# Optimization experiments

Hardware: AMD Instinct MI355X
Metric: run time of the kernel (lower is better)

## Reference

```python
import math
import jax, jax.numpy as jnp
import numpy as np

NUM_HEADS = 32
NUM_KV_HEADS = 8
HEAD_DIM = 128
HIDDEN = 4096
ROPE_THETA = 500000.0
ROPE_FACTOR = 8.0
HIGH_FF = 4.0
LOW_FF = 1.0
ORIG_MAX_POS = 8192


def _llama3_inv_freq():
    # Llama-3 rope frequency scaling
    inv = 1.0 / (ROPE_THETA ** (np.arange(0, HEAD_DIM, 2, dtype=np.float32) / HEAD_DIM))
    wavelen = 2.0 * np.pi / inv
    low_wl = ORIG_MAX_POS / LOW_FF
    high_wl = ORIG_MAX_POS / HIGH_FF
    inv_scaled = np.where(wavelen > low_wl, inv / ROPE_FACTOR, inv)
    smooth = (ORIG_MAX_POS / wavelen - LOW_FF) / (HIGH_FF - LOW_FF)
    smoothed = (1.0 - smooth) / ROPE_FACTOR * inv + smooth * inv
    is_medium = (wavelen <= low_wl) & (wavelen >= high_wl)
    return jnp.asarray(np.where(is_medium, smoothed, inv_scaled), dtype=jnp.float32)


def _rotate_half(x):
    h = x.shape[-1] // 2
    return jnp.concatenate([-x[..., h:], x[..., :h]], axis=-1)


def setup_inputs() -> dict:
    key = jax.random.key(0)
    ks = jax.random.split(key, 5)
    s = 0.02
    return {
        "x": jax.random.normal(ks[0], (1, 2048, HIDDEN), dtype=jnp.float32),
        "Wq": jax.random.normal(ks[1], (NUM_HEADS * HEAD_DIM, HIDDEN), dtype=jnp.float32) * s,
        "Wk": jax.random.normal(ks[2], (NUM_KV_HEADS * HEAD_DIM, HIDDEN), dtype=jnp.float32) * s,
        "Wv": jax.random.normal(ks[3], (NUM_KV_HEADS * HEAD_DIM, HIDDEN), dtype=jnp.float32) * s,
        "Wo": jax.random.normal(ks[4], (HIDDEN, NUM_HEADS * HEAD_DIM), dtype=jnp.float32) * s,
    }


def reference(x, Wq, Wk, Wv, Wo):
    B, T, _ = x.shape
    G = NUM_HEADS // NUM_KV_HEADS  # query heads per kv head

    q = jnp.einsum("bth,oh->bto", x, Wq).reshape(B, T, NUM_HEADS, HEAD_DIM).transpose(0, 2, 1, 3)
    k = jnp.einsum("bth,oh->bto", x, Wk).reshape(B, T, NUM_KV_HEADS, HEAD_DIM).transpose(0, 2, 1, 3)
    v = jnp.einsum("bth,oh->bto", x, Wv).reshape(B, T, NUM_KV_HEADS, HEAD_DIM).transpose(0, 2, 1, 3)

    # RoPE (past_len = 0, prefill)
    inv_freq = _llama3_inv_freq()
    pos = jnp.arange(T, dtype=jnp.float32)
    freqs = pos[:, None] * inv_freq[None, :]             # [T, D/2]
    emb = jnp.concatenate([freqs, freqs], axis=-1)       # [T, D]
    cos, sin = jnp.cos(emb), jnp.sin(emb)
    q = q * cos + _rotate_half(q) * sin
    k = k * cos + _rotate_half(k) * sin

    # GQA attention: group query heads over kv heads instead of repeat_interleave
    qg = q.reshape(B, NUM_KV_HEADS, G, T, HEAD_DIM)
    scale = 1.0 / math.sqrt(HEAD_DIM)
    scores = jnp.einsum("bkgtd,bksd->bkgts", qg, k) * scale  # [B,Hkv,G,T,T]
    causal = jnp.tril(jnp.ones((T, T), dtype=bool))
    scores = jnp.where(causal, scores, -jnp.inf)
    attn = jax.nn.softmax(scores, axis=-1)
    out = jnp.einsum("bkgts,bksd->bkgtd", attn, v)           # [B,Hkv,G,T,D]
    out = out.reshape(B, NUM_HEADS, T, HEAD_DIM).transpose(0, 2, 1, 3).reshape(B, T, NUM_HEADS * HEAD_DIM)
    return jnp.einsum("bto,ho->bth", out, Wo)
```

## Files before the change

### kernel.cpp

```cpp
#include <hip/hip_runtime.h>
#include <math.h>

#define T 2048
#define HID 4096
#define NH 32
#define NKV 8
#define HD 128
#define QSCALE 0.08838834764831845f

typedef __attribute__((ext_vector_type(8))) short short8;
typedef __attribute__((ext_vector_type(4))) float f32x4;
typedef __attribute__((ext_vector_type(16))) float f32x16;

static __device__ __forceinline__ unsigned short f2bf(float f) {
  union { float f; unsigned u; } v; v.f = f;
  unsigned r = v.u;
  r += 0x7fffu + ((r >> 16) & 1u);
  return (unsigned short)(r >> 16);
}

static __device__ __forceinline__ void async_cp16(const unsigned short* g, unsigned short* l) {
  __builtin_amdgcn_global_load_lds(
      (const __attribute__((address_space(1))) void*)g,
      (__attribute__((address_space(3))) void*)l,
      16, 0, 0);
}

__global__ __launch_bounds__(256) void cast4_kernel(const float* __restrict__ s0, const float* __restrict__ s1,
                                                    const float* __restrict__ s2, const float* __restrict__ s3,
                                                    unsigned short* __restrict__ d0, unsigned short* __restrict__ d1,
                                                    unsigned short* __restrict__ d2, unsigned short* __restrict__ d3,
                                                    int n0, int n1, int n2, int n3) {
  int i = blockIdx.x * 256 + threadIdx.x;
  const float* s; unsigned short* d; int j = i;
  if (j < n0) { s = s0; d = d0; }
  else { j -= n0;
    if (j < n1) { s = s1; d = d1; }
    else { j -= n1;
      if (j < n2) { s = s2; d = d2; }
      else { j -= n2;
        if (j >= n3) return;
        s = s3; d = d3; } } }
  float4 f = ((const float4*)s)[j];
  ushort4 o;
  o.x = f2bf(f.x); o.y = f2bf(f.y); o.z = f2bf(f.z); o.w = f2bf(f.w);
  ((ushort4*)d)[j] = o;
}

__global__ __launch_bounds__(256) void cast_bf16_kernel(const float* __restrict__ src,
                                                        unsigned short* __restrict__ dst,
                                                        int n4) {
  int i = blockIdx.x * 256 + threadIdx.x;
  if (i >= n4) return;
  float4 f = ((const float4*)src)[i];
  ushort4 o;
  o.x = f2bf(f.x); o.y = f2bf(f.y); o.z = f2bf(f.z); o.w = f2bf(f.w);
  ((ushort4*)dst)[i] = o;
}


static __device__ __forceinline__ short8 ldfrag(const unsigned short* tile, int row0, int ks, int lane) {
  int row = row0 + (lane & 15);
  int slot = (ks * 4 + (lane >> 4)) ^ (lane & 7);
  return *(const short8*)&tile[row * 64 + slot * 8];
}

static __device__ __forceinline__ void stage_half(const unsigned short* __restrict__ G, long grow0, int K, int k0,
                                                  unsigned short* lds, int h, int wave, int lane) {
#pragma unroll
  for (int i = 0; i < 2; i++) {
    long row = grow0 + h * 128 + i * 64 + wave * 8 + (lane >> 3);
    int slot = (lane & 7) ^ (lane >> 3);
    async_cp16(&G[row * (long)K + k0 + slot * 8], &lds[h * 8192 + i * 4096 + wave * 512]);
  }
}

template <int MQ, int NQ>
static __device__ __forceinline__ void mfma_quad(const short8 (&af)[4][2], const short8 (&bf)[2][2],
                                                 f32x4 (&acc)[8][4]) {
  __builtin_amdgcn_s_setprio(1);
#pragma unroll
  for (int m = 0; m < 4; m++)
#pragma unroll
    for (int n = 0; n < 2; n++)
#pragma unroll
      for (int ks = 0; ks < 2; ks++)
        acc[MQ * 4 + m][NQ * 2 + n] = __builtin_amdgcn_mfma_f32_16x16x32_bf16(
            af[m][ks], bf[n][ks], acc[MQ * 4 + m][NQ * 2 + n], 0, 0, 0);
  __builtin_amdgcn_s_setprio(0);
}

#define SCHED0 __builtin_amdgcn_sched_barrier(0)
#define BAR_PRE  do { SCHED0; __builtin_amdgcn_s_barrier(); \
                      asm volatile("s_waitcnt lgkmcnt(0)" ::: "memory"); SCHED0; } while (0)
#define BAR_POST do { SCHED0; __builtin_amdgcn_s_barrier(); SCHED0; } while (0)

__global__ __launch_bounds__(512, 2) void gemm8(const unsigned short* __restrict__ A,
                                                const unsigned short* __restrict__ Bt,
                                                float* __restrict__ C,
                                                int M, int N, int K) {
  __shared__ __align__(16) unsigned short As[2][16384];
  __shared__ __align__(16) unsigned short Bs[2][16384];
  int tid = threadIdx.x, wave = tid >> 6, lane = tid & 63;
  int wm = wave >> 2, wn = wave & 3;
  long bm0 = (long)blockIdx.y * 256, bn0 = (long)blockIdx.x * 256;
  int ar = wm * 128, br = wn * 64;

  f32x4 acc[8][4] = {};
  short8 a0[4][2], a1[4][2], b0[2][2], b1[2][2];

  stage_half(Bt, bn0, K, 0, Bs[0], 0, wave, lane);
  stage_half(Bt, bn0, K, 0, Bs[0], 1, wave, lane);
  stage_half(A,  bm0, K, 0, As[0], 0, wave, lane);
  stage_half(A,  bm0, K, 0, As[0], 1, wave, lane);
  stage_half(Bt, bn0, K, 64, Bs[1], 0, wave, lane);
  stage_half(Bt, bn0, K, 64, Bs[1], 1, wave, lane);
  asm volatile("s_waitcnt vmcnt(4)" ::: "memory");
  SCHED0; __builtin_amdgcn_s_barrier(); SCHED0;

  int nkt = K >> 6;
#pragma unroll 1
  for (int it = 0; it < (nkt >> 1); ++it) {
    int k1 = (2 * it + 1) << 6;
    int t2 = 2 * it + 2; if (t2 > nkt - 1) t2 = nkt - 1;
    int t3 = 2 * it + 3; if (t3 > nkt - 1) t3 = nkt - 1;
    int k2 = t2 << 6, k3 = t3 << 6;

#pragma unroll
    for (int m = 0; m < 4; m++)
#pragma unroll
      for (int ks = 0; ks < 2; ks++) a0[m][ks] = ldfrag(As[0], ar + m * 16, ks, lane);
#pragma unroll
    for (int n = 0; n < 2; n++)
#pragma unroll
      for (int ks = 0; ks < 2; ks++) b0[n][ks] = ldfrag(Bs[0], br + n * 16, ks, lane);
    stage_half(A, bm0, K, k1, As[1], 0, wave, lane);
    BAR_PRE; mfma_quad<0, 0>(a0, b0, acc); BAR_POST;

#pragma unroll
    for (int n = 0; n < 2; n++)
#pragma unroll
      for (int ks = 0; ks < 2; ks++) b1[n][ks] = ldfrag(Bs[0], br + (2 + n) * 16, ks, lane);
    stage_half(A, bm0, K, k1, As[1], 1, wave, lane);
    BAR_PRE; mfma_quad<0, 1>(a0, b1, acc); BAR_POST;

#pragma unroll
    for (int m = 0; m < 4; m++)
#pragma unroll
      for (int ks = 0; ks < 2; ks++) a1[m][ks] = ldfrag(As[0], ar + (4 + m) * 16, ks, lane);
    stage_half(Bt, bn0, K, k2, Bs[0], 0, wave, lane);
    BAR_PRE; mfma_quad<1, 0>(a1, b0, acc); BAR_POST;

    stage_half(Bt, bn0, K, k2, Bs[0], 1, wave, lane);
    asm volatile("s_waitcnt vmcnt(4)" ::: "memory");
    BAR_PRE; mfma_quad<1, 1>(a1, b1, acc); BAR_POST;

#pragma unroll
    for (int m = 0; m < 4; m++)
#pragma unroll
      for (int ks = 0; ks < 2; ks++) a0[m][ks] = ldfrag(As[1], ar + m * 16, ks, lane);
#pragma unroll
    for (int n = 0; n < 2; n++)
#pragma unroll
      for (int ks = 0; ks < 2; ks++) b0[n][ks] = ldfrag(Bs[1], br + n * 16, ks, lane);
    stage_half(A, bm0, K, k2, As[0], 0, wave, lane);
    BAR_PRE; mfma_quad<0, 0>(a0, b0, acc); BAR_POST;

#pragma unroll
    for (int n = 0; n < 2; n++)
#pragma unroll
      for (int ks = 0; ks < 2; ks++) b1[n][ks] = ldfrag(Bs[1], br + (2 + n) * 16, ks, lane);
    stage_half(A, bm0, K, k2, As[0], 1, wave, lane);
    BAR_PRE; mfma_quad<0, 1>(a0, b1, acc); BAR_POST;

#pragma unroll
    for (int m = 0; m < 4; m++)
#pragma unroll
      for (int ks = 0; ks < 2; ks++) a1[m][ks] = ldfrag(As[1], ar + (4 + m) * 16, ks, lane);
    stage_half(Bt, bn0, K, k3, Bs[1], 0, wave, lane);
    BAR_PRE; mfma_quad<1, 0>(a1, b0, acc); BAR_POST;

    stage_half(Bt, bn0, K, k3, Bs[1], 1, wave, lane);
    asm volatile("s_waitcnt vmcnt(4)" ::: "memory");
    BAR_PRE; mfma_quad<1, 1>(a1, b1, acc); BAR_POST;
  }
  asm volatile("s_waitcnt vmcnt(0)" ::: "memory");

#pragma unroll
  for (int m = 0; m < 8; m++)
#pragma unroll
    for (int n = 0; n < 4; n++) {
      long row = bm0 + ar + m * 16 + ((lane >> 4) << 2);
      long col = bn0 + br + n * 16 + (lane & 15);
#pragma unroll
      for (int j = 0; j < 4; j++)
        C[(row + j) * (long)N + col] = acc[m][n][j];
    }
}

__global__ __launch_bounds__(64) void rope_qk(const float* __restrict__ qkvf,
                                              unsigned short* __restrict__ qb,
                                              unsigned short* __restrict__ kb) {
  int t = blockIdx.x, hh = blockIdx.y, d = threadIdx.x;
  float ex = (float)d * (1.0f / 64.0f);
  float inv = expf(-ex * 13.122363377404328f);
  float wl = 6.283185307179586f / inv;
  float inv_s;
  if (wl > 8192.0f)       inv_s = inv * 0.125f;
  else if (wl < 2048.0f)  inv_s = inv;
  else {
    float smooth = (8192.0f / wl - 1.0f) * (1.0f / 3.0f);
    inv_s = (1.0f - smooth) * 0.125f * inv + smooth * inv;
  }
  float ang = (float)t * inv_s;
  float s, c;
  sincosf(ang, &s, &c);
  if (hh < NH) {
    const float* base = qkvf + (long)t * 6144 + hh * HD;
    float lo = base[d], hi = base[d + 64];
    long o = ((long)hh * T + t) * HD;
    qb[o + d]      = f2bf((lo * c - hi * s) * QSCALE);
    qb[o + d + 64] = f2bf((hi * c + lo * s) * QSCALE);
  } else {
    int h = hh - NH;
    const float* base = qkvf + (long)t * 6144 + 4096 + h * HD;
    float lo = base[d], hi = base[d + 64];
    long o = ((long)h * T + t) * HD;
    kb[o + d]      = f2bf(lo * c - hi * s);
    kb[o + d + 64] = f2bf(hi * c + lo * s);
  }
}

__global__ __launch_bounds__(256) void transpose_v(const float* __restrict__ qkvf,
                                                   unsigned short* __restrict__ vtb) {
  __shared__ float tile[64][33];
  int t0 = blockIdx.x * 64, d0 = blockIdx.y * 32, h = blockIdx.z;
  int tid = threadIdx.x;
  int dd = tid & 31, tt = tid >> 5;
#pragma unroll
  for (int i = 0; i < 8; i++) {
    int t = tt + i * 8;
    tile[t][dd] = qkvf[(long)(t0 + t) * 6144 + 5120 + h * HD + d0 + dd];
  }
  __syncthreads();
  int t2 = tid & 63, d2 = tid >> 6;
#pragma unroll
  for (int i = 0; i < 8; i++) {
    int d = d2 + i * 4;
    vtb[((long)(h * HD + d0 + d)) * T + t0 + t2] = f2bf(tile[t2][d]);
  }
}

__global__ __launch_bounds__(256, 2) void attn_kernel(const unsigned short* __restrict__ qb,
                                                      const unsigned short* __restrict__ kbuf,
                                                      const unsigned short* __restrict__ vtb,
                                                      unsigned short* __restrict__ ob) {
  __shared__ __align__(16) unsigned short Ks[64 * 128];
  __shared__ __align__(16) unsigned short Vs[128 * 64];
  __shared__ __align__(16) unsigned short Ps[4][32 * 76];
  int h = blockIdx.y;
  int kvh = h >> 2;
  int qt = (blockIdx.y >= 16) ? (int)(gridDim.x - 1 - blockIdx.x) : (int)blockIdx.x;
  int q0 = qt * 128;
  int tid = threadIdx.x, wave = tid >> 6, lane = tid & 63;
  int l31 = lane & 31, half = lane >> 5;
  const unsigned short* Kb = kbuf + (long)kvh * T * HD;
  const unsigned short* Vb = vtb + (long)kvh * HD * T;

  int qrow = q0 + wave * 32 + l31;
  short8 aq[8];
#pragma unroll
  for (int ks = 0; ks < 8; ks++)
    aq[ks] = *(const short8*)&qb[((long)h * T + qrow) * HD + ks * 16 + half * 8];

  f32x16 oacc[4] = {};
  float psum[16];
#pragma unroll
  for (int r = 0; r < 16; r++) psum[r] = 0.0f;

  int ntiles = 2 * qt + 2;
  for (int tile = 0; tile < ntiles; tile++) {
    int kb0 = tile * 64;
#pragma unroll
    for (int i = 0; i < 4; i++) {
      int c = wave * 4 + i;
      { int row = c * 4 + (lane >> 4);
        int g = (lane & 15) ^ (row & 15);
        async_cp16(&Kb[(long)(kb0 + row) * HD + g * 8], &Ks[c * 512]); }
      { int row = c * 8 + (lane >> 3);
        int g = (lane & 7) ^ (row & 7);
        async_cp16(&Vb[(long)row * T + kb0 + g * 8], &Vs[c * 512]); }
    }
    __syncthreads();

    f32x16 sacc[2] = {};
#pragma unroll
    for (int ks = 0; ks < 8; ks++)
#pragma unroll
      for (int nt = 0; nt < 2; nt++) {
        int row = nt * 32 + l31;
        short8 bk = *(const short8*)&Ks[row * 128 + (((2 * ks + half) ^ (row & 15)) * 8)];
        sacc[nt] = __builtin_amdgcn_mfma_f32_32x32x16_bf16(aq[ks], bk, sacc[nt], 0, 0, 0);
      }

    if (kb0 + 63 > q0 + wave * 32) {
#pragma unroll
      for (int nt = 0; nt < 2; nt++) {
        int key = kb0 + nt * 32 + l31;
#pragma unroll
        for (int r = 0; r < 16; r++) {
          int qr = q0 + wave * 32 + (r & 3) + 8 * (r >> 2) + 4 * half;
          if (key > qr) sacc[nt][r] = -3.0e38f;
        }
      }
    }

#pragma unroll
    for (int nt = 0; nt < 2; nt++)
#pragma unroll
      for (int r = 0; r < 16; r++) {
        float p = __expf(sacc[nt][r]);
        psum[r] += p;
        int prow = (r & 3) + 8 * (r >> 2) + 4 * half;
        Ps[wave][prow * 76 + nt * 32 + l31] = f2bf(p);
      }

#pragma unroll
    for (int ks = 0; ks < 4; ks++) {
      short8 ap = *(const short8*)&Ps[wave][l31 * 76 + ks * 16 + half * 8];
#pragma unroll
      for (int nt = 0; nt < 4; nt++) {
        int row = nt * 32 + l31;
        short8 bv = *(const short8*)&Vs[row * 64 + (((2 * ks + half) ^ (row & 7)) * 8)];
        oacc[nt] = __builtin_amdgcn_mfma_f32_32x32x16_bf16(ap, bv, oacc[nt], 0, 0, 0);
      }
    }
    __syncthreads();
  }

#pragma unroll
  for (int off = 1; off <= 16; off <<= 1)
#pragma unroll
    for (int r = 0; r < 16; r++)
      psum[r] += __shfl_xor(psum[r], off, 64);

#pragma unroll
  for (int nt = 0; nt < 4; nt++)
#pragma unroll
    for (int r = 0; r < 16; r++) {
      int row = q0 + wave * 32 + (r & 3) + 8 * (r >> 2) + 4 * half;
      ob[(long)row * HID + h * HD + nt * 32 + l31] = f2bf(oacc[nt][r] / psum[r]);
    }
}

extern "C" void kernel_launch(void* const* d_in, const int* in_sizes, int n_in,
                              void* d_out, int out_size, void* d_ws, size_t ws_size,
                              hipStream_t stream) {
  const float* x  = (const float*)d_in[0];
  const float* Wq = (const float*)d_in[1];
  const float* Wk = (const float*)d_in[2];
  const float* Wv = (const float*)d_in[3];
  const float* Wo = (const float*)d_in[4];
  float* out = (float*)d_out;

  char* ws = (char*)d_ws;
  size_t off = 0;
  auto alloc = [&](size_t bytes) {
    char* p = ws + off;
    off += (bytes + 255) & ~(size_t)255;
    return p;
  };
  unsigned short* x_bf    = (unsigned short*)alloc((size_t)T * HID * 2);
  unsigned short* wqkv_bf = (unsigned short*)alloc((size_t)6144 * HID * 2);
  float* qkvf = (float*)alloc((size_t)T * 6144 * 4);
  unsigned short* qb  = (unsigned short*)alloc((size_t)NH * T * HD * 2);
  unsigned short* kbb = (unsigned short*)alloc((size_t)NKV * T * HD * 2);
  unsigned short* vtb = (unsigned short*)alloc((size_t)NKV * HD * T * 2);
  unsigned short* obb = (unsigned short*)alloc((size_t)T * HID * 2);

  int n0 = T * HID / 4, n1 = HID * HID / 4, n2 = 1024 * HID / 4, n3 = 1024 * HID / 4;
  int ntot = n0 + n1 + n2 + n3;
  cast4_kernel<<<dim3((ntot + 255) / 256), dim3(256), 0, stream>>>(
      x, Wq, Wk, Wv,
      x_bf, wqkv_bf, wqkv_bf + (size_t)HID * HID, wqkv_bf + (size_t)5120 * HID,
      n0, n1, n2, n3);

  gemm8<<<dim3(6144 / 256, T / 256), dim3(512), 0, stream>>>(x_bf, wqkv_bf, qkvf, T, 6144, HID);

  rope_qk<<<dim3(T, NH + NKV), dim3(64), 0, stream>>>(qkvf, qb, kbb);
  transpose_v<<<dim3(T / 64, HD / 32, NKV), dim3(256), 0, stream>>>(qkvf, vtb);

  cast_bf16_kernel<<<dim3((HID * HID / 4 + 255) / 256), dim3(256), 0, stream>>>(Wo, wqkv_bf, HID * HID / 4);
  attn_kernel<<<dim3(T / 128, NH), dim3(256), 0, stream>>>(qb, kbb, vtb, obb);
  gemm8<<<dim3(HID / 256, T / 256), dim3(512), 0, stream>>>(obb, wqkv_bf, out, T, HID, HID);
}
```

Measured before the change: 506.8 us.

## Narrow GEMM N-tiles to fill all CUs with templated pipeline

Templates the bf16 GEMM on the number of N fragments per wave, giving 192-wide tiles for the QKV projection and 128-wide tiles for the output projection. The grids become 256 workgroups, matching the CU count, where before the projections launched 192 and 128 workgroups and left CUs idle. The staging and MFMA phase schedule is rebuilt per tile width with new vmcnt waits. Smaller N tiles lower the reuse of each loaded A tile and increase total global/L2 traffic.

```diff
diff --git a/kernel.cpp b/kernel.cpp
--- a/kernel.cpp
+++ b/kernel.cpp
@@ -65,28 +65,43 @@
   return *(const short8*)&tile[row * 64 + slot * 8];
 }
 
-static __device__ __forceinline__ void stage_half(const unsigned short* __restrict__ G, long grow0, int K, int k0,
-                                                  unsigned short* lds, int h, int wave, int lane) {
-#pragma unroll
-  for (int i = 0; i < 2; i++) {
-    long row = grow0 + h * 128 + i * 64 + wave * 8 + (lane >> 3);
-    int slot = (lane & 7) ^ (lane >> 3);
-    async_cp16(&G[row * (long)K + k0 + slot * 8], &lds[h * 8192 + i * 4096 + wave * 512]);
-  }
-}
-
-template <int MQ, int NQ>
-static __device__ __forceinline__ void mfma_quad(const short8 (&af)[4][2], const short8 (&bf)[2][2],
-                                                 f32x4 (&acc)[8][4]) {
+static __device__ __forceinline__ void stage64(const unsigned short* __restrict__ G, long grow0, int K, int k0,
+                                               unsigned short* lds, int wave, int lane) {
+  long row = grow0 + wave * 8 + (lane >> 3);
+  int slot = (lane & 7) ^ (lane >> 3);
+  async_cp16(&G[row * (long)K + k0 + slot * 8], &lds[wave * 512]);
+}
+
+template <int MQ>
+static __device__ __forceinline__ void lda(short8 (&dst)[4][2], const unsigned short* tile, int ar, int lane) {
+#pragma unroll
+  for (int m = 0; m < 4; m++)
+#pragma unroll
+    for (int ks = 0; ks < 2; ks++)
+      dst[m][ks] = ldfrag(tile, ar + MQ * 64 + m * 16, ks, lane);
+}
+
+template <int N0, int NN, int NF>
+static __device__ __forceinline__ void ldb(short8 (&b)[NF][2], const unsigned short* tile, int br, int lane) {
+#pragma unroll
+  for (int n = 0; n < NN; n++)
+#pragma unroll
+    for (int ks = 0; ks < 2; ks++)
+      b[N0 + n][ks] = ldfrag(tile, br + (N0 + n) * 16, ks, lane);
+}
+
+template <int MQ, int N0, int NN, int NF>
+static __device__ __forceinline__ void mfma_ph(const short8 (&af)[4][2], const short8 (&b)[NF][2],
+                                               f32x4 (&acc)[8][NF]) {
   __builtin_amdgcn_s_setprio(1);
 #pragma unroll
-  for (int m = 0; m < 4; m++)
-#pragma unroll
-    for (int n = 0; n < 2; n++)
-#pragma unroll
-      for (int ks = 0; ks < 2; ks++)
-        acc[MQ * 4 + m][NQ * 2 + n] = __builtin_amdgcn_mfma_f32_16x16x32_bf16(
-            af[m][ks], bf[n][ks], acc[MQ * 4 + m][NQ * 2 + n], 0, 0, 0);
+  for (int ks = 0; ks < 2; ks++)
+#pragma unroll
+    for (int m = 0; m < 4; m++)
+#pragma unroll
+      for (int n = 0; n < NN; n++)
+        acc[MQ * 4 + m][N0 + n] = __builtin_amdgcn_mfma_f32_16x16x32_bf16(
+            af[m][ks], b[N0 + n][ks], acc[MQ * 4 + m][N0 + n], 0, 0, 0);
   __builtin_amdgcn_s_setprio(0);
 }
 
@@ -94,102 +109,116 @@
 #define BAR_PRE  do { SCHED0; __builtin_amdgcn_s_barrier(); \
                       asm volatile("s_waitcnt lgkmcnt(0)" ::: "memory"); SCHED0; } while (0)
 #define BAR_POST do { SCHED0; __builtin_amdgcn_s_barrier(); SCHED0; } while (0)
-
-__global__ __launch_bounds__(512, 2) void gemm8(const unsigned short* __restrict__ A,
-                                                const unsigned short* __restrict__ Bt,
-                                                float* __restrict__ C,
-                                                int M, int N, int K) {
+#define VMCNT(n) asm volatile("s_waitcnt vmcnt(" #n ")" ::: "memory")
+
+template <int NF>
+__global__ __launch_bounds__(512, 2) void gemm8t(const unsigned short* __restrict__ A,
+                                                 const unsigned short* __restrict__ Bt,
+                                                 float* __restrict__ C,
+                                                 int M, int N, int K) {
+  constexpr int BN = NF * 64;
   __shared__ __align__(16) unsigned short As[2][16384];
-  __shared__ __align__(16) unsigned short Bs[2][16384];
+  __shared__ __align__(16) unsigned short Bs[2][BN * 64];
   int tid = threadIdx.x, wave = tid >> 6, lane = tid & 63;
   int wm = wave >> 2, wn = wave & 3;
-  long bm0 = (long)blockIdx.y * 256, bn0 = (long)blockIdx.x * 256;
-  int ar = wm * 128, br = wn * 64;
-
-  f32x4 acc[8][4] = {};
-  short8 a0[4][2], a1[4][2], b0[2][2], b1[2][2];
-
-  stage_half(Bt, bn0, K, 0, Bs[0], 0, wave, lane);
-  stage_half(Bt, bn0, K, 0, Bs[0], 1, wave, lane);
-  stage_half(A,  bm0, K, 0, As[0], 0, wave, lane);
-  stage_half(A,  bm0, K, 0, As[0], 1, wave, lane);
-  stage_half(Bt, bn0, K, 64, Bs[1], 0, wave, lane);
-  stage_half(Bt, bn0, K, 64, Bs[1], 1, wave, lane);
-  asm volatile("s_waitcnt vmcnt(4)" ::: "memory");
-  SCHED0; __builtin_amdgcn_s_barrier(); SCHED0;
-
+  long bm0 = (long)blockIdx.y * 256, bn0 = (long)blockIdx.x * BN;
+  int ar = wm * 128, br = wn * (NF * 16);
+
+  f32x4 acc[8][NF] = {};
+  short8 a0[4][2], a1[4][2], b[NF][2];
   int nkt = K >> 6;
+
+  if constexpr (NF == 3) {
+#pragma unroll
+    for (int c = 0; c < 3; c++) stage64(Bt, bn0 + c * 64, K, 0, &Bs[0][c * 4096], wave, lane);
+#pragma unroll
+    for (int c = 0; c < 4; c++) stage64(A, bm0 + c * 64, K, 0, &As[0][c * 4096], wave, lane);
+#pragma unroll
+    for (int c = 0; c < 3; c++) stage64(Bt, bn0 + c * 64, K, 64, &Bs[1][c * 4096], wave, lane);
+    VMCNT(3);
+    SCHED0; __builtin_amdgcn_s_barrier(); SCHED0;
+
 #pragma unroll 1
-  for (int it = 0; it < (nkt >> 1); ++it) {
-    int k1 = (2 * it + 1) << 6;
-    int t2 = 2 * it + 2; if (t2 > nkt - 1) t2 = nkt - 1;
-    int t3 = 2 * it + 3; if (t3 > nkt - 1) t3 = nkt - 1;
-    int k2 = t2 << 6, k3 = t3 << 6;
-
-#pragma unroll
-    for (int m = 0; m < 4; m++)
-#pragma unroll
-      for (int ks = 0; ks < 2; ks++) a0[m][ks] = ldfrag(As[0], ar + m * 16, ks, lane);
-#pragma unroll
-    for (int n = 0; n < 2; n++)
-#pragma unroll
-      for (int ks = 0; ks < 2; ks++) b0[n][ks] = ldfrag(Bs[0], br + n * 16, ks, lane);
-    stage_half(A, bm0, K, k1, As[1], 0, wave, lane);
-    BAR_PRE; mfma_quad<0, 0>(a0, b0, acc); BAR_POST;
-
-#pragma unroll
-    for (int n = 0; n < 2; n++)
-#pragma unroll
-      for (int ks = 0; ks < 2; ks++) b1[n][ks] = ldfrag(Bs[0], br + (2 + n) * 16, ks, lane);
-    stage_half(A, bm0, K, k1, As[1], 1, wave, lane);
-    BAR_PRE; mfma_quad<0, 1>(a0, b1, acc); BAR_POST;
-
-#pragma unroll
-    for (int m = 0; m < 4; m++)
-#pragma unroll
-      for (int ks = 0; ks < 2; ks++) a1[m][ks] = ldfrag(As[0], ar + (4 + m) * 16, ks, lane);
-    stage_half(Bt, bn0, K, k2, Bs[0], 0, wave, lane);
-    BAR_PRE; mfma_quad<1, 0>(a1, b0, acc); BAR_POST;
-
-    stage_half(Bt, bn0, K, k2, Bs[0], 1, wave, lane);
-    asm volatile("s_waitcnt vmcnt(4)" ::: "memory");
-    BAR_PRE; mfma_quad<1, 1>(a1, b1, acc); BAR_POST;
-
-#pragma unroll
-    for (int m = 0; m < 4; m++)
-#pragma unroll
-      for (int ks = 0; ks < 2; ks++) a0[m][ks] = ldfrag(As[1], ar + m * 16, ks, lane);
-#pragma unroll
-    for (int n = 0; n < 2; n++)
-#pragma unroll
-      for (int ks = 0; ks < 2; ks++) b0[n][ks] = ldfrag(Bs[1], br + n * 16, ks, lane);
-    stage_half(A, bm0, K, k2, As[0], 0, wave, lane);
-    BAR_PRE; mfma_quad<0, 0>(a0, b0, acc); BAR_POST;
-
-#pragma unroll
-    for (int n = 0; n < 2; n++)
-#pragma unroll
-      for (int ks = 0; ks < 2; ks++) b1[n][ks] = ldfrag(Bs[1], br + (2 + n) * 16, ks, lane);
-    stage_half(A, bm0, K, k2, As[0], 1, wave, lane);
-    BAR_PRE; mfma_quad<0, 1>(a0, b1, acc); BAR_POST;
-
-#pragma unroll
-    for (int m = 0; m < 4; m++)
-#pragma unroll
-      for (int ks = 0; ks < 2; ks++) a1[m][ks] = ldfrag(As[1], ar + (4 + m) * 16, ks, lane);
-    stage_half(Bt, bn0, K, k3, Bs[1], 0, wave, lane);
-    BAR_PRE; mfma_quad<1, 0>(a1, b0, acc); BAR_POST;
-
-    stage_half(Bt, bn0, K, k3, Bs[1], 1, wave, lane);
-    asm volatile("s_waitcnt vmcnt(4)" ::: "memory");
-    BAR_PRE; mfma_quad<1, 1>(a1, b1, acc); BAR_POST;
-  }
-  asm volatile("s_waitcnt vmcnt(0)" ::: "memory");
+    for (int it = 0; it < (nkt >> 1); ++it) {
+      int k1 = (2 * it + 1) << 6;
+      int t2 = 2 * it + 2; if (t2 > nkt - 1) t2 = nkt - 1;
+      int t3 = 2 * it + 3; if (t3 > nkt - 1) t3 = nkt - 1;
+      int k2 = t2 << 6, k3 = t3 << 6;
+
+      lda<0>(a0, As[0], ar, lane); ldb<0, 2, NF>(b, Bs[0], br, lane);
+      stage64(A, bm0 + 0, K, k1, &As[1][0], wave, lane);
+      stage64(A, bm0 + 64, K, k1, &As[1][4096], wave, lane);
+      BAR_PRE; mfma_ph<0, 0, 2>(a0, b, acc); BAR_POST;
+      ldb<2, 1, NF>(b, Bs[0], br, lane);
+      stage64(A, bm0 + 128, K, k1, &As[1][8192], wave, lane);
+      stage64(A, bm0 + 192, K, k1, &As[1][12288], wave, lane);
+      BAR_PRE; mfma_ph<0, 2, 1>(a0, b, acc); BAR_POST;
+      lda<1>(a1, As[0], ar, lane);
+      stage64(Bt, bn0 + 0, K, k2, &Bs[0][0], wave, lane);
+      stage64(Bt, bn0 + 64, K, k2, &Bs[0][4096], wave, lane);
+      BAR_PRE; mfma_ph<1, 0, 2>(a1, b, acc); BAR_POST;
+      stage64(Bt, bn0 + 128, K, k2, &Bs[0][8192], wave, lane);
+      VMCNT(3);
+      BAR_PRE; mfma_ph<1, 2, 1>(a1, b, acc); BAR_POST;
+      lda<0>(a0, As[1], ar, lane); ldb<0, 2, NF>(b, Bs[1], br, lane);
+      stage64(A, bm0 + 0, K, k2, &As[0][0], wave, lane);
+      stage64(A, bm0 + 64, K, k2, &As[0][4096], wave, lane);
+      BAR_PRE; mfma_ph<0, 0, 2>(a0, b, acc); BAR_POST;
+      ldb<2, 1, NF>(b, Bs[1], br, lane);
+      stage64(A, bm0 + 128, K, k2, &As[0][8192], wave, lane);
+      stage64(A, bm0 + 192, K, k2, &As[0][12288], wave, lane);
+      BAR_PRE; mfma_ph<0, 2, 1>(a0, b, acc); BAR_POST;
+      lda<1>(a1, As[1], ar, lane);
+      stage64(Bt, bn0 + 0, K, k3, &Bs[1][0], wave, lane);
+      stage64(Bt, bn0 + 64, K, k3, &Bs[1][4096], wave, lane);
+      BAR_PRE; mfma_ph<1, 0, 2>(a1, b, acc); BAR_POST;
+      stage64(Bt, bn0 + 128, K, k3, &Bs[1][8192], wave, lane);
+      VMCNT(3);
+      BAR_PRE; mfma_ph<1, 2, 1>(a1, b, acc); BAR_POST;
+    }
+  } else {
+#pragma unroll
+    for (int c = 0; c < 2; c++) stage64(Bt, bn0 + c * 64, K, 0, &Bs[0][c * 4096], wave, lane);
+#pragma unroll
+    for (int c = 0; c < 4; c++) stage64(A, bm0 + c * 64, K, 0, &As[0][c * 4096], wave, lane);
+#pragma unroll
+    for (int c = 0; c < 2; c++) stage64(Bt, bn0 + c * 64, K, 64, &Bs[1][c * 4096], wave, lane);
+    VMCNT(2);
+    SCHED0; __builtin_amdgcn_s_barrier(); SCHED0;
+
+#pragma unroll 1
+    for (int it = 0; it < (nkt >> 1); ++it) {
+      int k1 = (2 * it + 1) << 6;
+      int t2 = 2 * it + 2; if (t2 > nkt - 1) t2 = nkt - 1;
+      int t3 = 2 * it + 3; if (t3 > nkt - 1) t3 = nkt - 1;
+      int k2 = t2 << 6, k3 = t3 << 6;
+
+      lda<0>(a0, As[0], ar, lane); ldb<0, 2, NF>(b, Bs[0], br, lane);
+#pragma unroll
+      for (int c = 0; c < 4; c++) stage64(A, bm0 + c * 64, K, k1, &As[1][c * 4096], wave, lane);
+      BAR_PRE; mfma_ph<0, 0, 2>(a0, b, acc); BAR_POST;
+      lda<1>(a1, As[0], ar, lane);
+#pragma unroll
+      for (int c = 0; c < 2; c++) stage64(Bt, bn0 + c * 64, K, k2, &Bs[0][c * 4096], wave, lane);
+      VMCNT(2);
+      BAR_PRE; mfma_ph<1, 0, 2>(a1, b, acc); BAR_POST;
+      lda<0>(a0, As[1], ar, lane); ldb<0, 2, NF>(b, Bs[1], br, lane);
+#pragma unroll
+      for (int c = 0; c < 4; c++) stage64(A, bm0 + c * 64, K, k2, &As[0][c * 4096], wave, lane);
+      BAR_PRE; mfma_ph<0, 0, 2>(a0, b, acc); BAR_POST;
+      lda<1>(a1, As[1], ar, lane);
+#pragma unroll
+      for (int c = 0; c < 2; c++) stage64(Bt, bn0 + c * 64, K, k3, &Bs[1][c * 4096], wave, lane);
+      VMCNT(2);
+      BAR_PRE; mfma_ph<1, 0, 2>(a1, b, acc); BAR_POST;
+    }
+  }
+  VMCNT(0);
 
 #pragma unroll
   for (int m = 0; m < 8; m++)
 #pragma unroll
-    for (int n = 0; n < 4; n++) {
+    for (int n = 0; n < NF; n++) {
       long row = bm0 + ar + m * 16 + ((lane >> 4) << 2);
       long col = bn0 + br + n * 16 + (lane & 15);
 #pragma unroll
@@ -385,12 +414,12 @@
       x_bf, wqkv_bf, wqkv_bf + (size_t)HID * HID, wqkv_bf + (size_t)5120 * HID,
       n0, n1, n2, n3);
 
-  gemm8<<<dim3(6144 / 256, T / 256), dim3(512), 0, stream>>>(x_bf, wqkv_bf, qkvf, T, 6144, HID);
+  gemm8t<3><<<dim3(6144 / 192, T / 256), dim3(512), 0, stream>>>(x_bf, wqkv_bf, qkvf, T, 6144, HID);
 
   rope_qk<<<dim3(T, NH + NKV), dim3(64), 0, stream>>>(qkvf, qb, kbb);
   transpose_v<<<dim3(T / 64, HD / 32, NKV), dim3(256), 0, stream>>>(qkvf, vtb);
 
   cast_bf16_kernel<<<dim3((HID * HID / 4 + 255) / 256), dim3(256), 0, stream>>>(Wo, wqkv_bf, HID * HID / 4);
   attn_kernel<<<dim3(T / 128, NH), dim3(256), 0, stream>>>(qb, kbb, vtb, obb);
-  gemm8<<<dim3(HID / 256, T / 256), dim3(512), 0, stream>>>(obb, wqkv_bf, out, T, HID, HID);
-}
+  gemm8t<2><<<dim3(HID / 128, T / 256), dim3(512), 0, stream>>>(obb, wqkv_bf, out, T, HID, HID);
+}
```

New measurement: 459.3 us. 9.4% less time.
